# Kernel optimization log

Measured on AMD Instinct MI355X. Metric: run time of the kernel, lower is better.

Reference implementation:

```python
import jax, jax.numpy as jnp
import numpy as np

TOP_K = 8


def setup_inputs() -> dict:
    key = jax.random.key(0)
    ks = jax.random.split(key, 5)
    T, H, I, E = 4096, 2048, 1024, 64
    s = 0.02
    return {
        "x": jax.random.normal(ks[0], (T, H), jnp.float32),
        "gate_w": jax.random.normal(ks[1], (E, H), jnp.float32) * s,
        "gate_b": jax.random.normal(ks[2], (E,), jnp.float32) * s,
        "fc1_w": jax.random.normal(ks[3], (E, 2 * I, H), jnp.float32) * s,
        "fc2_w": jax.random.normal(ks[4], (E, H, I), jnp.float32) * s,
    }


def reference(x, gate_w, gate_b, fc1_w, fc2_w):
    # Router: [T, E] logits, top-k, softmax over selected logits in fp32.
    E = gate_w.shape[0]
    logits = x @ gate_w.T + gate_b
    topk_logits, topk_idx = jax.lax.top_k(logits, TOP_K)
    w = jax.nn.softmax(topk_logits.astype(jnp.float32), axis=-1).astype(x.dtype)
    # Per-token combine weight for each expert: [T, E] (0 if expert not selected).
    comb = (jax.nn.one_hot(topk_idx, E, dtype=x.dtype) * w[..., None]).sum(axis=1)
    # Scan over experts: each step is one dense GEMM-GeGLU-GEMM with masked combine.
    def body(acc, ew):
        W1, W2, c = ew  # W1 [2I, H], W2 [H, I], c [T]
        h_full = x @ W1.T                       # [T, 2I]
        h, g = jnp.split(h_full, 2, axis=-1)
        a = jax.nn.gelu(h, approximate=False) * (g + 1.0)  # custom GeGLU
        y = a @ W2.T                            # [T, H]
        return acc + c[:, None] * y, None

    out0 = jnp.zeros_like(x)
    out, _ = jax.lax.scan(body, out0, (fc1_w, fc2_w, comb.T))
    return out
```

## Files before the change

### kernel.cpp

```cpp
#include <hip/hip_runtime.h>
#include <hip/hip_bf16.h>
#include <cfloat>
#include <math.h>

#define T_TOK 4096
#define H_DIM 2048
#define E_NUM 64
#define I_DIM 1024
#define TOPK  8
#define BM    256
#define BK    64
#define MAXT  192

typedef __attribute__((ext_vector_type(4))) float f32x4;
typedef __attribute__((ext_vector_type(8))) short bf16x8;
typedef __attribute__((ext_vector_type(4))) int   i32x4;

__device__ __forceinline__ unsigned short f2bf(float f) {
    union { float f; unsigned int u; } v; v.f = f;
    unsigned int r = v.u + 0x7FFFu + ((v.u >> 16) & 1u);
    return (unsigned short)(r >> 16);
}
__device__ __forceinline__ unsigned int pack2(float a, float b) {
    return (unsigned int)f2bf(a) | ((unsigned int)f2bf(b) << 16);
}
__device__ __forceinline__ float bf2f(unsigned short u) {
    union { unsigned int u; float f; } v; v.u = (unsigned int)u << 16; return v.f;
}
__device__ __forceinline__ int cvtpk(float lo, float hi) {
    int r; asm("v_cvt_pk_bf16_f32 %0, %1, %2" : "=v"(r) : "v"(lo), "v"(hi)); return r;
}
__device__ __forceinline__ void gload16(const void* g, void* l) {
    __builtin_amdgcn_global_load_lds((const __attribute__((address_space(1))) unsigned int*)g,
                                     (__attribute__((address_space(3))) unsigned int*)l, 16, 0, 0);
}
#define WAIT_VM4   do { asm volatile("s_waitcnt vmcnt(4)" ::: "memory"); __builtin_amdgcn_sched_barrier(0); } while(0)
#define WAIT_VM8   do { asm volatile("s_waitcnt vmcnt(8)" ::: "memory"); __builtin_amdgcn_sched_barrier(0); } while(0)
#define WAIT_VM0   do { asm volatile("s_waitcnt vmcnt(0)" ::: "memory"); __builtin_amdgcn_sched_barrier(0); } while(0)
#define WAIT_LGKM0 do { asm volatile("s_waitcnt lgkmcnt(0)" ::: "memory"); __builtin_amdgcn_sched_barrier(0); } while(0)
#define BAR __builtin_amdgcn_s_barrier()

__global__ __launch_bounds__(256)
void router_kernel(const float* __restrict__ x, const float* __restrict__ gw,
                   const float* __restrict__ gb, unsigned short* __restrict__ xb,
                   int* __restrict__ topk_idx, float* __restrict__ topk_w,
                   int* __restrict__ counts)
{
    const int t = blockIdx.x;
    const int tid = threadIdx.x;
    __shared__ float xs[H_DIM];
    __shared__ float logits[E_NUM];
    const float* xrow = x + (size_t)t * H_DIM;

    #pragma unroll
    for (int i = 0; i < 2; ++i) {
        int c = i * 1024 + tid * 4;
        f32x4 v = *(const f32x4*)(xrow + c);
        *(f32x4*)(xs + c) = v;
        uint2 pk; pk.x = pack2(v.x, v.y); pk.y = pack2(v.z, v.w);
        *(uint2*)(xb + (size_t)t * H_DIM + c) = pk;
    }
    __syncthreads();

    const int wave = tid >> 6, lane = tid & 63;
    for (int ee = 0; ee < 16; ++ee) {
        const int e = wave * 16 + ee;
        const float* g = gw + (size_t)e * H_DIM;
        float p = 0.f;
        #pragma unroll
        for (int i = 0; i < 8; ++i) {
            int c = (i * 64 + lane) * 4;
            f32x4 gv = *(const f32x4*)(g + c);
            f32x4 xv = *(const f32x4*)(xs + c);
            p += gv.x * xv.x + gv.y * xv.y + gv.z * xv.z + gv.w * xv.w;
        }
        #pragma unroll
        for (int s = 32; s > 0; s >>= 1) p += __shfl_xor(p, s, 64);
        if (lane == 0) logits[e] = p + gb[e];
    }
    __syncthreads();

    if (tid < 64) {
        float cur = logits[tid];
        float wv[TOPK]; int wi[TOPK];
        #pragma unroll
        for (int k = 0; k < TOPK; ++k) {
            float bv = cur; int bi = tid;
            #pragma unroll
            for (int s = 32; s > 0; s >>= 1) {
                float ov = __shfl_xor(bv, s, 64);
                int   oi = __shfl_xor(bi, s, 64);
                if (ov > bv || (ov == bv && oi < bi)) { bv = ov; bi = oi; }
            }
            wv[k] = bv; wi[k] = bi;
            if (tid == bi) cur = -FLT_MAX;
        }
        if (tid == 0) {
            float mx = wv[0], sum = 0.f, ex[TOPK];
            #pragma unroll
            for (int k = 0; k < TOPK; ++k) { ex[k] = expf(wv[k] - mx); sum += ex[k]; }
            #pragma unroll
            for (int k = 0; k < TOPK; ++k) {
                topk_idx[t * TOPK + k] = wi[k];
                topk_w[t * TOPK + k]   = ex[k] / sum;
                atomicAdd(&counts[wi[k]], 1);
            }
        }
    }
}

__global__ void scan_kernel(const int* __restrict__ counts, int* __restrict__ offsets,
                            int* __restrict__ cursors, int* __restrict__ tiles,
                            int* __restrict__ ntiles)
{
    if (threadIdx.x == 0) {
        int acc = 0, nt = 0;
        for (int e = 0; e < E_NUM; ++e) {
            offsets[e] = acc; cursors[e] = acc;
            int c = counts[e];
            for (int m = 0; m * BM < c; ++m) tiles[nt++] = (e << 16) | m;
            acc += c;
        }
        *ntiles = nt;
    }
}

__global__ void assign_kernel(const int* __restrict__ topk_idx, const float* __restrict__ topk_w,
                              int* __restrict__ cursors, int* __restrict__ tok_of,
                              int* __restrict__ pos_of)
{
    int i = blockIdx.x * 256 + threadIdx.x;
    if (i >= T_TOK * TOPK) return;
    int e = topk_idx[i];
    int pos = atomicAdd(&cursors[e], 1);
    tok_of[pos] = i >> 3;
    pos_of[i]   = pos;
}

__global__ __launch_bounds__(512, 1)
void gemm1_kernel(const unsigned short* __restrict__ xb, const float* __restrict__ fc1,
                  const int* __restrict__ counts, const int* __restrict__ offsets,
                  const int* __restrict__ tok_of, const int* __restrict__ tiles,
                  const int* __restrict__ ntiles, unsigned short* __restrict__ a_all)
{
    const int ty = blockIdx.y;
    if (ty >= *ntiles) return;
    const int code = tiles[ty];
    const int e = code >> 16, m0 = (code & 0xffff) * BM;
    const int cnt = counts[e], off = offsets[e];
    const int pn0 = blockIdx.x * 128;
    const float* W = fc1 + (size_t)e * (size_t)(2 * I_DIM) * H_DIM;

    __shared__ unsigned short sA[2][BM * BK];
    __shared__ unsigned short sB[2][BM * BK];
    __shared__ int sTok[BM];

    const int tid = threadIdx.x;
    if (tid < BM) {
        int m = m0 + tid;
        sTok[tid] = tok_of[off + (m < cnt ? m : cnt - 1)];
    }
    __syncthreads();

    const int wid = tid >> 6, lane = tid & 63;
    const int srow = tid >> 3, sch = tid & 7;
    const int brow = tid >> 1, bhalf = tid & 1;

    const unsigned short* aSrc[4];
    #pragma unroll
    for (int i = 0; i < 4; ++i) {
        int row = srow + 64 * i;
        aSrc[i] = xb + (size_t)sTok[row] * H_DIM + (sch ^ (row & 7)) * 8;
    }
    const int wrow = (brow < 128) ? (pn0 + brow) : (I_DIM + pn0 + (brow - 128));
    const float* bSrc = W + (size_t)wrow * H_DIM + bhalf * 32;

    f32x4 accH[8][2], accG[8][2];
    #pragma unroll
    for (int m = 0; m < 8; ++m)
        #pragma unroll
        for (int n = 0; n < 2; ++n) {
            accH[m][n] = (f32x4){0.f, 0.f, 0.f, 0.f};
            accG[m][n] = (f32x4){0.f, 0.f, 0.f, 0.f};
        }

    const int wm = (wid >> 2) * 128;
    const int wn = (wid & 3) * 32;
    const int fr = lane & 15;
    const int kg = lane >> 4;

    f32x4 br[8];

    auto loadB = [&](int k0) {
        #pragma unroll
        for (int j = 0; j < 8; ++j) br[j] = *(const f32x4*)(bSrc + k0 + j * 4);
    };
    auto issueA = [&](int k0, int buf) {
        #pragma unroll
        for (int i = 0; i < 4; ++i)
            gload16(aSrc[i] + k0, &sA[buf][i * 4096 + tid * 8]);
    };
    auto storeB = [&](int buf) {
        #pragma unroll
        for (int j = 0; j < 4; ++j) {
            i32x4 pk = (i32x4){cvtpk(br[2*j].x,   br[2*j].y),
                               cvtpk(br[2*j].z,   br[2*j].w),
                               cvtpk(br[2*j+1].x, br[2*j+1].y),
                               cvtpk(br[2*j+1].z, br[2*j+1].w)};
            int s = bhalf * 4 + j;
            *(i32x4*)((char*)sB[buf] + brow * 128 + ((s ^ (brow & 7)) * 16)) = pk;
        }
    };
    auto compute = [&](int buf) {
        #pragma unroll
        for (int kk = 0; kk < 2; ++kk) {
            bf16x8 af[8], bh[2], bg[2];
            #pragma unroll
            for (int m = 0; m < 8; ++m) {
                int row = wm + m * 16 + fr;
                af[m] = *(const bf16x8*)((const char*)sA[buf] +
                        row * 128 + (((kk * 4 + kg) ^ (row & 7)) * 16));
            }
            #pragma unroll
            for (int n = 0; n < 2; ++n) {
                int rh = wn + n * 16 + fr;
                bh[n] = *(const bf16x8*)((const char*)sB[buf] +
                        rh * 128 + (((kk * 4 + kg) ^ (rh & 7)) * 16));
                int rg = 128 + rh;
                bg[n] = *(const bf16x8*)((const char*)sB[buf] +
                        rg * 128 + (((kk * 4 + kg) ^ (rg & 7)) * 16));
            }
            __builtin_amdgcn_s_setprio(1);
            #pragma unroll
            for (int m = 0; m < 8; ++m)
                #pragma unroll
                for (int n = 0; n < 2; ++n) {
                    accH[m][n] = __builtin_amdgcn_mfma_f32_16x16x32_bf16(af[m], bh[n], accH[m][n], 0, 0, 0);
                    accG[m][n] = __builtin_amdgcn_mfma_f32_16x16x32_bf16(af[m], bg[n], accG[m][n], 0, 0, 0);
                }
            __builtin_amdgcn_s_setprio(0);
        }
    };

    const int NT = H_DIM / BK;
    loadB(0);
    issueA(0, 0);
    WAIT_VM4;
    storeB(0);
    loadB(BK);
    WAIT_VM8;
    WAIT_LGKM0;
    BAR;

    int cur = 0;
    #pragma unroll 1
    for (int t = 0; t < NT; ++t) {
        const bool n1 = (t + 1) < NT, n2 = (t + 2) < NT;
        if (n1) {
            issueA((t + 1) * BK, cur ^ 1);
            WAIT_VM4;
            storeB(cur ^ 1);
        }
        if (n2) loadB((t + 2) * BK);
        compute(cur);
        if (n2)      { WAIT_VM8; }
        else if (n1) { WAIT_VM0; }
        WAIT_LGKM0;
        BAR;
        cur ^= 1;
    }

    #pragma unroll
    for (int m = 0; m < 8; ++m) {
        int rbase = wm + m * 16 + kg * 4;
        #pragma unroll
        for (int r = 0; r < 4; ++r) {
            int gm = m0 + rbase + r;
            if (gm < cnt) {
                size_t rowoff = (size_t)(off + gm) * I_DIM + pn0 + wn;
                #pragma unroll
                for (int n = 0; n < 2; ++n) {
                    float h = accH[m][n][r];
                    float g = accG[m][n][r];
                    float a = 0.5f * h * (1.f + erff(h * 0.70710678118f)) * (g + 1.f);
                    a_all[rowoff + n * 16 + fr] = f2bf(a);
                }
            }
        }
    }
}

__global__ __launch_bounds__(512, 1)
void gemm2_kernel(const unsigned short* __restrict__ a_all, const float* __restrict__ fc2,
                  const int* __restrict__ counts, const int* __restrict__ offsets,
                  const int* __restrict__ tiles, const int* __restrict__ ntiles,
                  unsigned short* __restrict__ y)
{
    const int ty = blockIdx.y;
    if (ty >= *ntiles) return;
    const int code = tiles[ty];
    const int e = code >> 16, m0 = (code & 0xffff) * BM;
    const int cnt = counts[e], off = offsets[e];
    const int n0 = blockIdx.x * 256;
    const float* W = fc2 + (size_t)e * (size_t)H_DIM * I_DIM;

    __shared__ unsigned short sA[2][BM * BK];
    __shared__ unsigned short sB[2][BM * BK];

    const int tid = threadIdx.x;
    const int wid = tid >> 6, lane = tid & 63;
    const int srow = tid >> 3, sch = tid & 7;
    const int brow = tid >> 1, bhalf = tid & 1;

    const unsigned short* aSrc[4];
    #pragma unroll
    for (int i = 0; i < 4; ++i) {
        int row = srow + 64 * i;
        aSrc[i] = a_all + (size_t)(off + m0 + row) * I_DIM + (sch ^ (row & 7)) * 8;
    }
    const float* bSrc = W + (size_t)(n0 + brow) * I_DIM + bhalf * 32;

    f32x4 acc[8][4];
    #pragma unroll
    for (int m = 0; m < 8; ++m)
        #pragma unroll
        for (int n = 0; n < 4; ++n) acc[m][n] = (f32x4){0.f, 0.f, 0.f, 0.f};

    const int wm = (wid >> 2) * 128;
    const int wn = (wid & 3) * 64;
    const int fr = lane & 15;
    const int kg = lane >> 4;

    f32x4 br[8];

    auto loadB = [&](int k0) {
        #pragma unroll
        for (int j = 0; j < 8; ++j) br[j] = *(const f32x4*)(bSrc + k0 + j * 4);
    };
    auto issueA = [&](int k0, int buf) {
        #pragma unroll
        for (int i = 0; i < 4; ++i)
            gload16(aSrc[i] + k0, &sA[buf][i * 4096 + tid * 8]);
    };
    auto storeB = [&](int buf) {
        #pragma unroll
        for (int j = 0; j < 4; ++j) {
            i32x4 pk = (i32x4){cvtpk(br[2*j].x,   br[2*j].y),
                               cvtpk(br[2*j].z,   br[2*j].w),
                               cvtpk(br[2*j+1].x, br[2*j+1].y),
                               cvtpk(br[2*j+1].z, br[2*j+1].w)};
            int s = bhalf * 4 + j;
            *(i32x4*)((char*)sB[buf] + brow * 128 + ((s ^ (brow & 7)) * 16)) = pk;
        }
    };
    auto compute = [&](int buf) {
        #pragma unroll
        for (int kk = 0; kk < 2; ++kk) {
            bf16x8 af[8], bf[4];
            #pragma unroll
            for (int m = 0; m < 8; ++m) {
                int row = wm + m * 16 + fr;
                af[m] = *(const bf16x8*)((const char*)sA[buf] +
                        row * 128 + (((kk * 4 + kg) ^ (row & 7)) * 16));
            }
            #pragma unroll
            for (int n = 0; n < 4; ++n) {
                int row = wn + n * 16 + fr;
                bf[n] = *(const bf16x8*)((const char*)sB[buf] +
                        row * 128 + (((kk * 4 + kg) ^ (row & 7)) * 16));
            }
            __builtin_amdgcn_s_setprio(1);
            #pragma unroll
            for (int m = 0; m < 8; ++m)
                #pragma unroll
                for (int n = 0; n < 4; ++n)
                    acc[m][n] = __builtin_amdgcn_mfma_f32_16x16x32_bf16(af[m], bf[n], acc[m][n], 0, 0, 0);
            __builtin_amdgcn_s_setprio(0);
        }
    };

    const int NT = I_DIM / BK;
    loadB(0);
    issueA(0, 0);
    WAIT_VM4;
    storeB(0);
    loadB(BK);
    WAIT_VM8;
    WAIT_LGKM0;
    BAR;

    int cur = 0;
    #pragma unroll 1
    for (int t = 0; t < NT; ++t) {
        const bool n1 = (t + 1) < NT, n2 = (t + 2) < NT;
        if (n1) {
            issueA((t + 1) * BK, cur ^ 1);
            WAIT_VM4;
            storeB(cur ^ 1);
        }
        if (n2) loadB((t + 2) * BK);
        compute(cur);
        if (n2)      { WAIT_VM8; }
        else if (n1) { WAIT_VM0; }
        WAIT_LGKM0;
        BAR;
        cur ^= 1;
    }

    #pragma unroll
    for (int m = 0; m < 8; ++m) {
        int rbase = wm + m * 16 + kg * 4;
        #pragma unroll
        for (int r = 0; r < 4; ++r) {
            int gm = m0 + rbase + r;
            if (gm < cnt) {
                size_t rowoff = (size_t)(off + gm) * H_DIM + n0 + wn;
                #pragma unroll
                for (int n = 0; n < 4; ++n)
                    y[rowoff + n * 16 + fr] = f2bf(acc[m][n][r]);
            }
        }
    }
}

__global__ __launch_bounds__(256)
void combine_kernel(const unsigned short* __restrict__ y, const int* __restrict__ pos_of,
                    const float* __restrict__ topk_w, float* __restrict__ out)
{
    const int t = blockIdx.x;
    const int tid = threadIdx.x;
    __shared__ int   sp[TOPK];
    __shared__ float sw[TOPK];
    if (tid < TOPK) {
        sp[tid] = pos_of[t * TOPK + tid];
        sw[tid] = topk_w[t * TOPK + tid];
    }
    __syncthreads();

    const int c0 = tid * 8;
    float acc[8];
    #pragma unroll
    for (int j = 0; j < 8; ++j) acc[j] = 0.f;
    #pragma unroll
    for (int k = 0; k < TOPK; ++k) {
        const float w = sw[k];
        i32x4 v = *(const i32x4*)(y + (size_t)sp[k] * H_DIM + c0);
        const unsigned short* u = (const unsigned short*)&v;
        #pragma unroll
        for (int j = 0; j < 8; ++j) acc[j] += w * bf2f(u[j]);
    }
    float* orow = out + (size_t)t * H_DIM + c0;
    *(f32x4*)orow       = (f32x4){acc[0], acc[1], acc[2], acc[3]};
    *(f32x4*)(orow + 4) = (f32x4){acc[4], acc[5], acc[6], acc[7]};
}

extern "C" void kernel_launch(void* const* d_in, const int* in_sizes, int n_in,
                              void* d_out, int out_size, void* d_ws, size_t ws_size,
                              hipStream_t stream)
{
    const float* x   = (const float*)d_in[0];
    const float* gw  = (const float*)d_in[1];
    const float* gb  = (const float*)d_in[2];
    const float* fc1 = (const float*)d_in[3];
    const float* fc2 = (const float*)d_in[4];
    float* out = (float*)d_out;

    char* ws = (char*)d_ws;
    size_t o = 0;
    auto alloc = [&](size_t b) { void* p = ws + o; o = (o + b + 255) & ~(size_t)255; return p; };
    unsigned short* xb     = (unsigned short*)alloc((size_t)T_TOK * H_DIM * 2);
    int*            tk_idx = (int*)  alloc((size_t)T_TOK * TOPK * 4);
    float*          tk_w   = (float*)alloc((size_t)T_TOK * TOPK * 4);
    int*            counts = (int*)  alloc(E_NUM * 4);
    int*            offs   = (int*)  alloc(E_NUM * 4);
    int*            curs   = (int*)  alloc(E_NUM * 4);
    int*            tiles  = (int*)  alloc(MAXT * 4);
    int*            ntiles = (int*)  alloc(4);
    int*            tok_of = (int*)  alloc((size_t)T_TOK * TOPK * 4);
    int*            pos_of = (int*)  alloc((size_t)T_TOK * TOPK * 4);
    unsigned short* a_all  = (unsigned short*)alloc((size_t)(T_TOK * TOPK + BM) * I_DIM * 2);
    unsigned short* yb     = (unsigned short*)alloc((size_t)(T_TOK * TOPK + BM) * H_DIM * 2);
    (void)ws_size;

    hipMemsetAsync(counts, 0, E_NUM * 4, stream);

    router_kernel<<<T_TOK, 256, 0, stream>>>(x, gw, gb, xb, tk_idx, tk_w, counts);
    scan_kernel<<<1, 64, 0, stream>>>(counts, offs, curs, tiles, ntiles);
    assign_kernel<<<(T_TOK * TOPK + 255) / 256, 256, 0, stream>>>(tk_idx, tk_w, curs, tok_of, pos_of);
    gemm1_kernel<<<dim3(I_DIM / 128, MAXT), 512, 0, stream>>>(xb, fc1, counts, offs, tok_of,
                                                              tiles, ntiles, a_all);
    gemm2_kernel<<<dim3(H_DIM / 256, MAXT), 512, 0, stream>>>(a_all, fc2, counts, offs,
                                                              tiles, ntiles, yb);
    combine_kernel<<<T_TOK, 256, 0, stream>>>(yb, pos_of, tk_w, out);
}
```

Measured before the change: 1.313 ms.

## Shrink GEMM tiles to 256 threads and BK=32 for two blocks per CU

Both grouped GEMM kernels move from 512-thread blocks with 256x256 (or 256x128) tiles and BK=64 to 256-thread blocks with half-width N tiles and BK=32. The LDS swizzle is changed to a 4-chunk XOR pattern to fit the new row layout, and the wait counts are adjusted. The aim is to fit two blocks per CU so that memory latency hides better and more N blocks spread over the CUs. The cost is that each weight row and each gathered A row is reloaded twice as often, with twice as many barriers per K step and less reuse per block.

```diff
diff --git a/kernel.cpp b/kernel.cpp
--- a/kernel.cpp
+++ b/kernel.cpp
@@ -9,7 +9,7 @@
 #define I_DIM 1024
 #define TOPK  8
 #define BM    256
-#define BK    64
+#define BK    32
 #define MAXT  192
 
 typedef __attribute__((ext_vector_type(4))) float f32x4;
@@ -34,8 +34,9 @@
     __builtin_amdgcn_global_load_lds((const __attribute__((address_space(1))) unsigned int*)g,
                                      (__attribute__((address_space(3))) unsigned int*)l, 16, 0, 0);
 }
+__device__ __forceinline__ int xr(int row) { return (row & 3) ^ ((row >> 2) & 3); }
+
 #define WAIT_VM4   do { asm volatile("s_waitcnt vmcnt(4)" ::: "memory"); __builtin_amdgcn_sched_barrier(0); } while(0)
-#define WAIT_VM8   do { asm volatile("s_waitcnt vmcnt(8)" ::: "memory"); __builtin_amdgcn_sched_barrier(0); } while(0)
 #define WAIT_VM0   do { asm volatile("s_waitcnt vmcnt(0)" ::: "memory"); __builtin_amdgcn_sched_barrier(0); } while(0)
 #define WAIT_LGKM0 do { asm volatile("s_waitcnt lgkmcnt(0)" ::: "memory"); __builtin_amdgcn_sched_barrier(0); } while(0)
 #define BAR __builtin_amdgcn_s_barrier()
@@ -137,7 +138,7 @@
     pos_of[i]   = pos;
 }
 
-__global__ __launch_bounds__(512, 1)
+__global__ __launch_bounds__(256, 2)
 void gemm1_kernel(const unsigned short* __restrict__ xb, const float* __restrict__ fc1,
                   const int* __restrict__ counts, const int* __restrict__ offsets,
                   const int* __restrict__ tok_of, const int* __restrict__ tiles,
@@ -148,32 +149,29 @@
     const int code = tiles[ty];
     const int e = code >> 16, m0 = (code & 0xffff) * BM;
     const int cnt = counts[e], off = offsets[e];
-    const int pn0 = blockIdx.x * 128;
+    const int pn0 = blockIdx.x * 64;
     const float* W = fc1 + (size_t)e * (size_t)(2 * I_DIM) * H_DIM;
 
     __shared__ unsigned short sA[2][BM * BK];
-    __shared__ unsigned short sB[2][BM * BK];
+    __shared__ unsigned short sB[2][128 * BK];
     __shared__ int sTok[BM];
 
     const int tid = threadIdx.x;
-    if (tid < BM) {
-        int m = m0 + tid;
-        sTok[tid] = tok_of[off + (m < cnt ? m : cnt - 1)];
-    }
+    sTok[tid] = tok_of[off + ((m0 + tid) < cnt ? (m0 + tid) : cnt - 1)];
     __syncthreads();
 
     const int wid = tid >> 6, lane = tid & 63;
-    const int srow = tid >> 3, sch = tid & 7;
+    const int srow = tid >> 2, sch = tid & 3;
     const int brow = tid >> 1, bhalf = tid & 1;
 
     const unsigned short* aSrc[4];
     #pragma unroll
     for (int i = 0; i < 4; ++i) {
         int row = srow + 64 * i;
-        aSrc[i] = xb + (size_t)sTok[row] * H_DIM + (sch ^ (row & 7)) * 8;
-    }
-    const int wrow = (brow < 128) ? (pn0 + brow) : (I_DIM + pn0 + (brow - 128));
-    const float* bSrc = W + (size_t)wrow * H_DIM + bhalf * 32;
+        aSrc[i] = xb + (size_t)sTok[row] * H_DIM + (sch ^ xr(row)) * 8;
+    }
+    const int wrow = (brow < 64) ? (pn0 + brow) : (I_DIM + pn0 + (brow - 64));
+    const float* bSrc = W + (size_t)wrow * H_DIM + bhalf * 16;
 
     f32x4 accH[8][2], accG[8][2];
     #pragma unroll
@@ -184,62 +182,56 @@
             accG[m][n] = (f32x4){0.f, 0.f, 0.f, 0.f};
         }
 
-    const int wm = (wid >> 2) * 128;
-    const int wn = (wid & 3) * 32;
+    const int wm = (wid >> 1) * 128;
+    const int wnp = (wid & 1) * 32;
     const int fr = lane & 15;
     const int kg = lane >> 4;
 
-    f32x4 br[8];
+    f32x4 br[4];
 
     auto loadB = [&](int k0) {
         #pragma unroll
-        for (int j = 0; j < 8; ++j) br[j] = *(const f32x4*)(bSrc + k0 + j * 4);
+        for (int j = 0; j < 4; ++j) br[j] = *(const f32x4*)(bSrc + k0 + j * 4);
     };
     auto issueA = [&](int k0, int buf) {
         #pragma unroll
         for (int i = 0; i < 4; ++i)
-            gload16(aSrc[i] + k0, &sA[buf][i * 4096 + tid * 8]);
+            gload16(aSrc[i] + k0, &sA[buf][i * 2048 + tid * 8]);
     };
     auto storeB = [&](int buf) {
         #pragma unroll
-        for (int j = 0; j < 4; ++j) {
+        for (int j = 0; j < 2; ++j) {
             i32x4 pk = (i32x4){cvtpk(br[2*j].x,   br[2*j].y),
                                cvtpk(br[2*j].z,   br[2*j].w),
                                cvtpk(br[2*j+1].x, br[2*j+1].y),
                                cvtpk(br[2*j+1].z, br[2*j+1].w)};
-            int s = bhalf * 4 + j;
-            *(i32x4*)((char*)sB[buf] + brow * 128 + ((s ^ (brow & 7)) * 16)) = pk;
+            int s = bhalf * 2 + j;
+            *(i32x4*)((char*)sB[buf] + brow * 64 + ((s ^ xr(brow)) * 16)) = pk;
         }
     };
     auto compute = [&](int buf) {
-        #pragma unroll
-        for (int kk = 0; kk < 2; ++kk) {
-            bf16x8 af[8], bh[2], bg[2];
-            #pragma unroll
-            for (int m = 0; m < 8; ++m) {
-                int row = wm + m * 16 + fr;
-                af[m] = *(const bf16x8*)((const char*)sA[buf] +
-                        row * 128 + (((kk * 4 + kg) ^ (row & 7)) * 16));
-            }
+        bf16x8 af[8], bh[2], bg[2];
+        #pragma unroll
+        for (int m = 0; m < 8; ++m) {
+            int row = wm + m * 16 + fr;
+            af[m] = *(const bf16x8*)((const char*)sA[buf] + row * 64 + ((kg ^ xr(row)) * 16));
+        }
+        #pragma unroll
+        for (int n = 0; n < 2; ++n) {
+            int rh = wnp + n * 16 + fr;
+            bh[n] = *(const bf16x8*)((const char*)sB[buf] + rh * 64 + ((kg ^ xr(rh)) * 16));
+            int rg = 64 + rh;
+            bg[n] = *(const bf16x8*)((const char*)sB[buf] + rg * 64 + ((kg ^ xr(rg)) * 16));
+        }
+        __builtin_amdgcn_s_setprio(1);
+        #pragma unroll
+        for (int m = 0; m < 8; ++m)
             #pragma unroll
             for (int n = 0; n < 2; ++n) {
-                int rh = wn + n * 16 + fr;
-                bh[n] = *(const bf16x8*)((const char*)sB[buf] +
-                        rh * 128 + (((kk * 4 + kg) ^ (rh & 7)) * 16));
-                int rg = 128 + rh;
-                bg[n] = *(const bf16x8*)((const char*)sB[buf] +
-                        rg * 128 + (((kk * 4 + kg) ^ (rg & 7)) * 16));
+                accH[m][n] = __builtin_amdgcn_mfma_f32_16x16x32_bf16(af[m], bh[n], accH[m][n], 0, 0, 0);
+                accG[m][n] = __builtin_amdgcn_mfma_f32_16x16x32_bf16(af[m], bg[n], accG[m][n], 0, 0, 0);
             }
-            __builtin_amdgcn_s_setprio(1);
-            #pragma unroll
-            for (int m = 0; m < 8; ++m)
-                #pragma unroll
-                for (int n = 0; n < 2; ++n) {
-                    accH[m][n] = __builtin_amdgcn_mfma_f32_16x16x32_bf16(af[m], bh[n], accH[m][n], 0, 0, 0);
-                    accG[m][n] = __builtin_amdgcn_mfma_f32_16x16x32_bf16(af[m], bg[n], accG[m][n], 0, 0, 0);
-                }
-            __builtin_amdgcn_s_setprio(0);
-        }
+        __builtin_amdgcn_s_setprio(0);
     };
 
     const int NT = H_DIM / BK;
@@ -248,7 +240,7 @@
     WAIT_VM4;
     storeB(0);
     loadB(BK);
-    WAIT_VM8;
+    WAIT_VM4;
     WAIT_LGKM0;
     BAR;
 
@@ -263,7 +255,7 @@
         }
         if (n2) loadB((t + 2) * BK);
         compute(cur);
-        if (n2)      { WAIT_VM8; }
+        if (n2)      { WAIT_VM4; }
         else if (n1) { WAIT_VM0; }
         WAIT_LGKM0;
         BAR;
@@ -277,7 +269,7 @@
         for (int r = 0; r < 4; ++r) {
             int gm = m0 + rbase + r;
             if (gm < cnt) {
-                size_t rowoff = (size_t)(off + gm) * I_DIM + pn0 + wn;
+                size_t rowoff = (size_t)(off + gm) * I_DIM + pn0 + wnp;
                 #pragma unroll
                 for (int n = 0; n < 2; ++n) {
                     float h = accH[m][n][r];
@@ -290,7 +282,7 @@
     }
 }
 
-__global__ __launch_bounds__(512, 1)
+__global__ __launch_bounds__(256, 2)
 void gemm2_kernel(const unsigned short* __restrict__ a_all, const float* __restrict__ fc2,
                   const int* __restrict__ counts, const int* __restrict__ offsets,
                   const int* __restrict__ tiles, const int* __restrict__ ntiles,
@@ -301,24 +293,24 @@
     const int code = tiles[ty];
     const int e = code >> 16, m0 = (code & 0xffff) * BM;
     const int cnt = counts[e], off = offsets[e];
-    const int n0 = blockIdx.x * 256;
+    const int n0 = blockIdx.x * 128;
     const float* W = fc2 + (size_t)e * (size_t)H_DIM * I_DIM;
 
     __shared__ unsigned short sA[2][BM * BK];
-    __shared__ unsigned short sB[2][BM * BK];
+    __shared__ unsigned short sB[2][128 * BK];
 
     const int tid = threadIdx.x;
     const int wid = tid >> 6, lane = tid & 63;
-    const int srow = tid >> 3, sch = tid & 7;
+    const int srow = tid >> 2, sch = tid & 3;
     const int brow = tid >> 1, bhalf = tid & 1;
 
     const unsigned short* aSrc[4];
     #pragma unroll
     for (int i = 0; i < 4; ++i) {
         int row = srow + 64 * i;
-        aSrc[i] = a_all + (size_t)(off + m0 + row) * I_DIM + (sch ^ (row & 7)) * 8;
-    }
-    const float* bSrc = W + (size_t)(n0 + brow) * I_DIM + bhalf * 32;
+        aSrc[i] = a_all + (size_t)(off + m0 + row) * I_DIM + (sch ^ xr(row)) * 8;
+    }
+    const float* bSrc = W + (size_t)(n0 + brow) * I_DIM + bhalf * 16;
 
     f32x4 acc[8][4];
     #pragma unroll
@@ -326,57 +318,52 @@
         #pragma unroll
         for (int n = 0; n < 4; ++n) acc[m][n] = (f32x4){0.f, 0.f, 0.f, 0.f};
 
-    const int wm = (wid >> 2) * 128;
-    const int wn = (wid & 3) * 64;
+    const int wm = (wid >> 1) * 128;
+    const int wn = (wid & 1) * 64;
     const int fr = lane & 15;
     const int kg = lane >> 4;
 
-    f32x4 br[8];
+    f32x4 br[4];
 
     auto loadB = [&](int k0) {
         #pragma unroll
-        for (int j = 0; j < 8; ++j) br[j] = *(const f32x4*)(bSrc + k0 + j * 4);
+        for (int j = 0; j < 4; ++j) br[j] = *(const f32x4*)(bSrc + k0 + j * 4);
     };
     auto issueA = [&](int k0, int buf) {
         #pragma unroll
         for (int i = 0; i < 4; ++i)
-            gload16(aSrc[i] + k0, &sA[buf][i * 4096 + tid * 8]);
+            gload16(aSrc[i] + k0, &sA[buf][i * 2048 + tid * 8]);
     };
     auto storeB = [&](int buf) {
         #pragma unroll
-        for (int j = 0; j < 4; ++j) {
+        for (int j = 0; j < 2; ++j) {
             i32x4 pk = (i32x4){cvtpk(br[2*j].x,   br[2*j].y),
                                cvtpk(br[2*j].z,   br[2*j].w),
                                cvtpk(br[2*j+1].x, br[2*j+1].y),
                                cvtpk(br[2*j+1].z, br[2*j+1].w)};
-            int s = bhalf * 4 + j;
-            *(i32x4*)((char*)sB[buf] + brow * 128 + ((s ^ (brow & 7)) * 16)) = pk;
+            int s = bhalf * 2 + j;
+            *(i32x4*)((char*)sB[buf] + brow * 64 + ((s ^ xr(brow)) * 16)) = pk;
         }
     };
     auto compute = [&](int buf) {
-        #pragma unroll
-        for (int kk = 0; kk < 2; ++kk) {
-            bf16x8 af[8], bf[4];
+        bf16x8 af[8], bf[4];
+        #pragma unroll
+        for (int m = 0; m < 8; ++m) {
+            int row = wm + m * 16 + fr;
+            af[m] = *(const bf16x8*)((const char*)sA[buf] + row * 64 + ((kg ^ xr(row)) * 16));
+        }
+        #pragma unroll
+        for (int n = 0; n < 4; ++n) {
+            int row = wn + n * 16 + fr;
+            bf[n] = *(const bf16x8*)((const char*)sB[buf] + row * 64 + ((kg ^ xr(row)) * 16));
+        }
+        __builtin_amdgcn_s_setprio(1);
+        #pragma unroll
+        for (int m = 0; m < 8; ++m)
             #pragma unroll
-            for (int m = 0; m < 8; ++m) {
-                int row = wm + m * 16 + fr;
-                af[m] = *(const bf16x8*)((const char*)sA[buf] +
-                        row * 128 + (((kk * 4 + kg) ^ (row & 7)) * 16));
-            }
-            #pragma unroll
-            for (int n = 0; n < 4; ++n) {
-                int row = wn + n * 16 + fr;
-                bf[n] = *(const bf16x8*)((const char*)sB[buf] +
-                        row * 128 + (((kk * 4 + kg) ^ (row & 7)) * 16));
-            }
-            __builtin_amdgcn_s_setprio(1);
-            #pragma unroll
-            for (int m = 0; m < 8; ++m)
-                #pragma unroll
-                for (int n = 0; n < 4; ++n)
-                    acc[m][n] = __builtin_amdgcn_mfma_f32_16x16x32_bf16(af[m], bf[n], acc[m][n], 0, 0, 0);
-            __builtin_amdgcn_s_setprio(0);
-        }
+            for (int n = 0; n < 4; ++n)
+                acc[m][n] = __builtin_amdgcn_mfma_f32_16x16x32_bf16(af[m], bf[n], acc[m][n], 0, 0, 0);
+        __builtin_amdgcn_s_setprio(0);
     };
 
     const int NT = I_DIM / BK;
@@ -385,7 +372,7 @@
     WAIT_VM4;
     storeB(0);
     loadB(BK);
-    WAIT_VM8;
+    WAIT_VM4;
     WAIT_LGKM0;
     BAR;
 
@@ -400,7 +387,7 @@
         }
         if (n2) loadB((t + 2) * BK);
         compute(cur);
-        if (n2)      { WAIT_VM8; }
+        if (n2)      { WAIT_VM4; }
         else if (n1) { WAIT_VM0; }
         WAIT_LGKM0;
         BAR;
@@ -487,9 +474,9 @@
     router_kernel<<<T_TOK, 256, 0, stream>>>(x, gw, gb, xb, tk_idx, tk_w, counts);
     scan_kernel<<<1, 64, 0, stream>>>(counts, offs, curs, tiles, ntiles);
     assign_kernel<<<(T_TOK * TOPK + 255) / 256, 256, 0, stream>>>(tk_idx, tk_w, curs, tok_of, pos_of);
-    gemm1_kernel<<<dim3(I_DIM / 128, MAXT), 512, 0, stream>>>(xb, fc1, counts, offs, tok_of,
-                                                              tiles, ntiles, a_all);
-    gemm2_kernel<<<dim3(H_DIM / 256, MAXT), 512, 0, stream>>>(a_all, fc2, counts, offs,
+    gemm1_kernel<<<dim3(I_DIM / 64, MAXT), 256, 0, stream>>>(xb, fc1, counts, offs, tok_of,
+                                                             tiles, ntiles, a_all);
+    gemm2_kernel<<<dim3(H_DIM / 128, MAXT), 256, 0, stream>>>(a_all, fc2, counts, offs,
                                                               tiles, ntiles, yb);
     combine_kernel<<<T_TOK, 256, 0, stream>>>(yb, pos_of, tk_w, out);
 }
```

Result: faster. 1.130 ms (median of 2 runs) (-13.9%).
